# Performance work log

Measured on AMD Instinct MI355X. Metric: run time of the kernel, lower is better.

The kernel has to match this reference:

```python
import jax, jax.numpy as jnp
import numpy as np
from jax import lax

NUM_CLASSES = 10
NUM_ITER = 3
DN = ('NCHW', 'OIHW', 'NCHW')


def squash(t, axis=-1):
    sq = (t ** 2).sum(axis=axis, keepdims=True)
    return (sq / (1.0 + sq)) * t / jnp.sqrt(sq)


def setup_inputs() -> dict:
    key = jax.random.key(0)
    ks = jax.random.split(key, 12)
    B = 512
    s = 0.05  # param scale for numerical stability
    return {
        'x': jax.random.normal(ks[0], (B, 1, 28, 28), jnp.float32),
        'conv1_w': jax.random.normal(ks[1], (256, 1, 9, 9), jnp.float32) * s,
        'conv1_b': jax.random.normal(ks[2], (256,), jnp.float32) * s,
        'prim_w': jax.random.normal(ks[3], (8, 32, 256, 9, 9), jnp.float32) * s,
        'prim_b': jax.random.normal(ks[4], (8, 32), jnp.float32) * s,
        'route_w': jax.random.normal(ks[5], (NUM_CLASSES, 32 * 6 * 6, 8, 16), jnp.float32),
        'dec_w1': jax.random.normal(ks[6], (512, 16 * NUM_CLASSES), jnp.float32) * s,
        'dec_b1': jax.random.normal(ks[7], (512,), jnp.float32) * s,
        'dec_w2': jax.random.normal(ks[8], (1024, 512), jnp.float32) * s,
        'dec_b2': jax.random.normal(ks[9], (1024,), jnp.float32) * s,
        'dec_w3': jax.random.normal(ks[10], (784, 1024), jnp.float32) * s,
        'dec_b3': jax.random.normal(ks[11], (784,), jnp.float32) * s,
    }


def reference(x, conv1_w, conv1_b, prim_w, prim_b, route_w,
              dec_w1, dec_b1, dec_w2, dec_b2, dec_w3, dec_b3):
    B = x.shape[0]
    # conv1 + relu: [B,256,20,20]
    h = lax.conv_general_dilated(x, conv1_w, (1, 1), 'VALID', dimension_numbers=DN)
    h = jax.nn.relu(h + conv1_b[None, :, None, None])
    # primary capsules: 8 parallel convs fused into one conv with 8*32 out channels
    kw = prim_w.reshape(8 * 32, 256, 9, 9)
    u = lax.conv_general_dilated(h, kw, (2, 2), 'VALID', dimension_numbers=DN)
    u = u + prim_b.reshape(-1)[None, :, None, None]          # [B,256,6,6]
    u = u.reshape(B, 8, 32 * 6 * 6).transpose(0, 2, 1)       # [B,1152,8]
    u = squash(u, axis=-1)
    # digit capsules: priors [C,B,R,16]
    priors = jnp.einsum('bri,crio->cbro', u, route_w)
    logits = jnp.zeros_like(priors)
    for i in range(NUM_ITER):
        probs = jax.nn.softmax(logits, axis=2)
        v = squash((probs * priors).sum(axis=2, keepdims=True))  # [C,B,1,16]
        if i != NUM_ITER - 1:
            logits = logits + (priors * v).sum(axis=-1, keepdims=True)
    caps = v.squeeze(2).transpose(1, 0, 2)                    # [B,C,16]
    classes = jnp.sqrt((caps ** 2).sum(axis=-1))              # [B,C]
    classes = jax.nn.softmax(classes, axis=1)
    y = jax.nn.one_hot(jnp.argmax(classes, axis=1), NUM_CLASSES, dtype=caps.dtype)
    d = (caps * y[:, :, None]).reshape(B, -1)                 # [B,160]
    d = jax.nn.relu(d @ dec_w1.T + dec_b1)
    d = jax.nn.relu(d @ dec_w2.T + dec_b2)
    recon = jax.nn.sigmoid(d @ dec_w3.T + dec_b3)             # [B,784]
    return classes, recon
```

## Files before the change

### kernel.cpp

```cpp
#include <hip/hip_runtime.h>
#include <math.h>


typedef _Float16 f16;
typedef _Float16 f16x8 __attribute__((ext_vector_type(8)));
typedef _Float16 f16x4 __attribute__((ext_vector_type(4)));
typedef float f32x4 __attribute__((ext_vector_type(4)));

__device__ __forceinline__ void gl_lds16(const void* g, void* l) {
  __builtin_amdgcn_global_load_lds(
      (const __attribute__((address_space(1))) void*)g,
      (__attribute__((address_space(3))) void*)l, 16, 0, 0);
}

__global__ __launch_bounds__(256, 2) void conv1_kernel(
    const float* __restrict__ x, const float* __restrict__ w,
    const float* __restrict__ bias, f16* __restrict__ ht)
{
  __shared__ float xs[784];
  const int b = blockIdx.x;
  const int t = threadIdx.x;
  for (int i = t; i < 784; i += 256) xs[i] = x[b * 784 + i];
  float wr[81];
#pragma unroll
  for (int k = 0; k < 81; ++k) wr[k] = w[t * 81 + k];
  const float bv = bias[t];
  __syncthreads();
  for (int oy = 0; oy < 20; ++oy) {
    float acc[20];
#pragma unroll
    for (int i = 0; i < 20; ++i) acc[i] = bv;
#pragma unroll
    for (int ky = 0; ky < 9; ++ky) {
      float xr[28];
#pragma unroll
      for (int q = 0; q < 7; ++q) {
        const float4 v = *(const float4*)&xs[(oy + ky) * 28 + q * 4];
        xr[q*4+0] = v.x; xr[q*4+1] = v.y; xr[q*4+2] = v.z; xr[q*4+3] = v.w;
      }
#pragma unroll
      for (int kx = 0; kx < 9; ++kx) {
        const float wv = wr[ky * 9 + kx];
#pragma unroll
        for (int ox = 0; ox < 20; ++ox) acc[ox] = fmaf(xr[ox + kx], wv, acc[ox]);
      }
    }
    f16* hp = &ht[(size_t)((b * 20 + oy) * 20) * 256 + t];
#pragma unroll
    for (int ox = 0; ox < 20; ++ox)
      hp[ox * 256] = (f16)fmaxf(acc[ox], 0.f);
  }
}

__global__ __launch_bounds__(256) void wtrans_kernel(
    const float* __restrict__ w, f16* __restrict__ wt)
{
  __shared__ float tile[64 * 83];
  const int oc = blockIdx.x;
  const int icq = blockIdx.y;
  const int t = threadIdx.x;
  const float* src = w + (size_t)oc * 20736 + (size_t)icq * 64 * 81;
  for (int idx = t; idx < 5184; idx += 256) {
    const int ici = idx / 81, kk = idx - ici * 81;
    tile[ici * 83 + kk] = src[idx];
  }
  __syncthreads();
  f16* dst = wt + (size_t)oc * 20736 + icq * 64;
  for (int idx = t; idx < 5184; idx += 256) {
    const int kk = idx >> 6, ici = idx & 63;
    dst[kk * 256 + ici] = (f16)tile[ici * 83 + kk];
  }
}

__global__ __launch_bounds__(256) void prim_mfma_kernel(
    const f16* __restrict__ ht, const f16* __restrict__ wt,
    float* __restrict__ part)
{
  __shared__ f16 sm[8192];
  const int t = threadIdx.x;
  const int wv = t >> 6, lane = t & 63;
  const int id = blockIdx.x;
  const int g = id >> 3;
  const int mb = (id & 7) + 8 * (g >> 2);
  const int nb = (g >> 1) & 1;
  const int ks = g & 1;
  const int m0 = mb * 128, n0 = nb * 128;

  const int chunk = (lane & 3) ^ ((lane >> 3) & 3);
  long aoff[2], boff[2];
#pragma unroll
  for (int i = 0; i < 2; ++i) {
    const int r = wv * 32 + i * 16 + (lane >> 2);
    const int m = m0 + r;
    const int b = m / 36, pos = m - b * 36;
    const int oy = pos / 6, ox = pos - oy * 6;
    aoff[i] = (long)(((b * 20 + 2 * oy) * 20 + 2 * ox) * 256) * 2 + chunk * 16;
    boff[i] = (long)(n0 + r) * 41472 + chunk * 16;
  }
  const char* htc = (const char*)ht;
  const char* wtc = (const char*)wt;

  const int lrow = lane & 15, quad = lane >> 4;
  const int qx = quad ^ ((lrow >> 1) & 3);
  const int wm = wv & 1, wn = wv >> 1;
  f32x4 acc[4][4] = {};

  const int s0 = ks * 324, s1 = s0 + 324;
  for (int s = s0; s < s1; ++s) {
    const int kykx = s >> 3, icb = s & 7;
    const int ky = kykx / 9, kx = kykx - ky * 9;
    const long astep = (long)((((ky * 20 + kx) * 256) + icb * 32) * 2);
    const long bstep = (long)(((kykx * 256) + icb * 32) * 2);
    __syncthreads();
    {
      char* dA = (char*)sm + wv * 2048;
      char* dB = (char*)sm + 8192 + wv * 2048;
      gl_lds16(htc + aoff[0] + astep, dA);
      gl_lds16(htc + aoff[1] + astep, dA + 1024);
      gl_lds16(wtc + boff[0] + bstep, dB);
      gl_lds16(wtc + boff[1] + bstep, dB + 1024);
    }
    __syncthreads();
    const f16* As = sm;
    const f16* Bs = sm + 4096;
    f16x8 af[4], bf[4];
#pragma unroll
    for (int mt = 0; mt < 4; ++mt)
      af[mt] = *(const f16x8*)&As[(wm * 64 + mt * 16 + lrow) * 32 + qx * 8];
#pragma unroll
    for (int nt = 0; nt < 4; ++nt)
      bf[nt] = *(const f16x8*)&Bs[(wn * 64 + nt * 16 + lrow) * 32 + qx * 8];
#pragma unroll
    for (int mt = 0; mt < 4; ++mt)
#pragma unroll
      for (int nt = 0; nt < 4; ++nt)
        acc[mt][nt] = __builtin_amdgcn_mfma_f32_16x16x32_f16(
            af[mt], bf[nt], acc[mt][nt], 0, 0, 0);
  }

  float* pp = part + (size_t)ks * 4718592;
#pragma unroll
  for (int mt = 0; mt < 4; ++mt) {
    const int mbase = m0 + wm * 64 + mt * 16 + quad * 4;
#pragma unroll
    for (int nt = 0; nt < 4; ++nt) {
      const int n = n0 + wn * 64 + nt * 16 + lrow;
      const int np = (n & 31) * 8 + (n >> 5);
#pragma unroll
      for (int rg = 0; rg < 4; ++rg)
        pp[(size_t)(mbase + rg) * 256 + np] = acc[mt][nt][rg];
    }
  }
}

__global__ void squash_kernel(const float* __restrict__ part,
                              const float* __restrict__ bias,
                              float* __restrict__ u)
{
  const int tid = blockIdx.x * 256 + threadIdx.x;
  if (tid >= 512 * 36 * 32) return;
  const int cc = tid & 31;
  const int row = tid >> 5;
  const int b = row / 36;
  const int pos = row - b * 36;
  const float* p = part + (size_t)row * 256 + cc * 8;
  float v[8] = {};
#pragma unroll
  for (int ksl = 0; ksl < 2; ++ksl) {
    const float4 a0 = *(const float4*)(p + (size_t)ksl * 4718592);
    const float4 a1 = *(const float4*)(p + (size_t)ksl * 4718592 + 4);
    v[0] += a0.x; v[1] += a0.y; v[2] += a0.z; v[3] += a0.w;
    v[4] += a1.x; v[5] += a1.y; v[6] += a1.z; v[7] += a1.w;
  }
  float sq = 0.f;
#pragma unroll
  for (int i = 0; i < 8; ++i) {
    v[i] += bias[i * 32 + cc];
    sq = fmaf(v[i], v[i], sq);
  }
  const float scale = sq / ((1.f + sq) * sqrtf(sq));
  float* up = &u[(size_t)(b * 1152 + cc * 36 + pos) * 8];
#pragma unroll
  for (int i = 0; i < 8; ++i) up[i] = v[i] * scale;
}

__global__ __launch_bounds__(256, 4) void priors_kernel(
    const float* __restrict__ u, const float* __restrict__ rw,
    f16* __restrict__ P)
{
  const int t = threadIdx.x;
  const int rl = t >> 2, oq = t & 3;
  const int r = blockIdx.x * 64 + rl;
  const int b0 = blockIdx.y * 64;
  const int c = blockIdx.z;

  float4 wreg[8];
  const float* wbase = rw + (size_t)(c * 1152 + r) * 128 + oq * 4;
#pragma unroll
  for (int k = 0; k < 8; ++k)
    wreg[k] = *(const float4*)(wbase + k * 16);

  f16* pbase = P + (size_t)((c * 512 + b0) * 1152 + r) * 16 + oq * 4;
  const float* ubase = u + (size_t)(b0 * 1152 + r) * 8;

  for (int b = 0; b < 64; ++b) {
    const float4 ua = *(const float4*)(ubase + (size_t)b * 9216);
    const float4 ub = *(const float4*)(ubase + (size_t)b * 9216 + 4);
    const float uu[8] = {ua.x, ua.y, ua.z, ua.w, ub.x, ub.y, ub.z, ub.w};
    float ax = 0.f, ay = 0.f, az = 0.f, aw = 0.f;
#pragma unroll
    for (int k = 0; k < 8; ++k) {
      ax = fmaf(uu[k], wreg[k].x, ax);
      ay = fmaf(uu[k], wreg[k].y, ay);
      az = fmaf(uu[k], wreg[k].z, az);
      aw = fmaf(uu[k], wreg[k].w, aw);
    }
    f16x4 st;
    st[0] = (f16)ax; st[1] = (f16)ay; st[2] = (f16)az; st[3] = (f16)aw;
    *(f16x4*)(pbase + (size_t)b * 18432) = st;
  }
}

__device__ __forceinline__ float wave_sum(float v) {
#pragma unroll
  for (int off = 32; off > 0; off >>= 1) v += __shfl_xor(v, off);
  return v;
}
__device__ __forceinline__ float wave_max(float v) {
#pragma unroll
  for (int off = 32; off > 0; off >>= 1) v = fmaxf(v, __shfl_xor(v, off));
  return v;
}

__global__ __launch_bounds__(256, 2) void routing_kernel(
    const f16* __restrict__ Pg, float* __restrict__ caps)
{
  const int c = blockIdx.x >> 9;
  const int b = blockIdx.x & 511;
  const int t = threadIdx.x;
  const int wid = t >> 6;
  const int lane = t & 63;
  __shared__ float xred[4 * 17];

  float P[5][16];
  float lg[5];
  const int nk = (t < 128) ? 5 : 4;
#pragma unroll
  for (int k = 0; k < 5; ++k)
#pragma unroll
    for (int o = 0; o < 16; ++o) P[k][o] = 0.f;

  const f16* pbase = Pg + (size_t)((c * 512 + b) * 1152) * 16;
#pragma unroll
  for (int k = 0; k < 5; ++k) {
    if (k < nk) {
      const int r = t + (k << 8);
      const f16x8 p0 = *(const f16x8*)&pbase[(size_t)r * 16];
      const f16x8 p1 = *(const f16x8*)&pbase[(size_t)r * 16 + 8];
#pragma unroll
      for (int o = 0; o < 8; ++o) {
        P[k][o]     = (float)p0[o];
        P[k][o + 8] = (float)p1[o];
      }
    }
  }

  float v[16];
  {
    float sq = 0.f;
#pragma unroll
    for (int o = 0; o < 16; ++o) {
      float p = 0.f;
#pragma unroll
      for (int k = 0; k < 5; ++k) p += P[k][o];
      p = wave_sum(p);
      if (lane == 0) xred[wid * 17 + o] = p;
      v[o] = 0.f;
    }
    __syncthreads();
#pragma unroll
    for (int o = 0; o < 16; ++o) {
      const float s = (xred[o] + xred[17 + o] + xred[34 + o] + xred[51 + o]) *
                      (1.f / 1152.f);
      v[o] = s;
      sq = fmaf(s, s, sq);
    }
    const float scale = sq / ((1.f + sq) * sqrtf(sq));
#pragma unroll
    for (int o = 0; o < 16; ++o) v[o] *= scale;
    __syncthreads();
  }
#pragma unroll
  for (int k = 0; k < 5; ++k) {
    float a = 0.f;
#pragma unroll
    for (int o = 0; o < 16; ++o) a = fmaf(P[k][o], v[o], a);
    lg[k] = a;
  }

  for (int it = 1; it < 3; ++it) {
    float m = -1e30f;
#pragma unroll
    for (int k = 0; k < 5; ++k) if (k < nk) m = fmaxf(m, lg[k]);
    m = wave_max(m);
    if (lane == 0) xred[wid * 17 + 16] = m;
    __syncthreads();
    const float mx = fmaxf(fmaxf(xred[16], xred[17 + 16]),
                           fmaxf(xred[34 + 16], xred[51 + 16]));
    __syncthreads();
    float e[5];
#pragma unroll
    for (int k = 0; k < 5; ++k) e[k] = (k < nk) ? expf(lg[k] - mx) : 0.f;
    float pS = 0.f;
#pragma unroll
    for (int k = 0; k < 5; ++k) pS += e[k];
    pS = wave_sum(pS);
    if (lane == 0) xred[wid * 17 + 16] = pS;
#pragma unroll
    for (int o = 0; o < 16; ++o) {
      float p = 0.f;
#pragma unroll
      for (int k = 0; k < 5; ++k) p = fmaf(e[k], P[k][o], p);
      p = wave_sum(p);
      if (lane == 0) xred[wid * 17 + o] = p;
    }
    __syncthreads();
    const float S = xred[16] + xred[17 + 16] + xred[34 + 16] + xred[51 + 16];
    const float inv = 1.f / S;
    float sq = 0.f;
#pragma unroll
    for (int o = 0; o < 16; ++o) {
      const float s = (xred[o] + xred[17 + o] + xred[34 + o] + xred[51 + o]) * inv;
      v[o] = s;
      sq = fmaf(s, s, sq);
    }
    const float scale = sq / ((1.f + sq) * sqrtf(sq));
#pragma unroll
    for (int o = 0; o < 16; ++o) v[o] *= scale;
    __syncthreads();
    if (it < 2) {
#pragma unroll
      for (int k = 0; k < 5; ++k) {
        float a = 0.f;
#pragma unroll
        for (int o = 0; o < 16; ++o) a = fmaf(P[k][o], v[o], a);
        lg[k] += a;
      }
    }
  }
  if (t == 0) {
    float* cp = &caps[(b * 10 + c) * 16];
#pragma unroll
    for (int o = 0; o < 16; ++o) cp[o] = v[o];
  }
}

__global__ void classes_kernel(const float* __restrict__ caps,
                               float* __restrict__ out_classes,
                               float* __restrict__ d0)
{
  const int b = blockIdx.x * 256 + threadIdx.x;
  if (b >= 512) return;
  float nrm[10];
#pragma unroll
  for (int cc = 0; cc < 10; ++cc) {
    float sq = 0.f;
#pragma unroll
    for (int o = 0; o < 16; ++o) {
      const float vv = caps[(b * 10 + cc) * 16 + o];
      sq = fmaf(vv, vv, sq);
    }
    nrm[cc] = sqrtf(sq);
  }
  float mx = nrm[0]; int cs = 0;
#pragma unroll
  for (int cc = 1; cc < 10; ++cc)
    if (nrm[cc] > mx) { mx = nrm[cc]; cs = cc; }
  float e[10], ssum = 0.f;
#pragma unroll
  for (int cc = 0; cc < 10; ++cc) { e[cc] = expf(nrm[cc] - mx); ssum += e[cc]; }
  const float inv = 1.f / ssum;
#pragma unroll
  for (int cc = 0; cc < 10; ++cc) out_classes[b * 10 + cc] = e[cc] * inv;
#pragma unroll
  for (int cc = 0; cc < 10; ++cc)
#pragma unroll
    for (int o = 0; o < 16; ++o)
      d0[b * 160 + cc * 16 + o] = (cc == cs) ? caps[(b * 10 + cc) * 16 + o] : 0.f;
}

__global__ __launch_bounds__(256, 2) void fc_kernel(
    const float* __restrict__ A, const float* __restrict__ W,
    const float* __restrict__ bias, float* __restrict__ C,
    int N, int K, int act)
{
  __shared__ float As[64][17];
  __shared__ float Ws[64][17];
  const int t = threadIdx.x;
  const int tm = t >> 4, tn = t & 15;
  const int m0 = blockIdx.y << 6, n0 = blockIdx.x << 6;
  const int lr = t >> 2, lq = (t & 3) << 2;
  float acc[4][4] = {};
  for (int k0 = 0; k0 < K; k0 += 16) {
    const float4 av = *(const float4*)&A[(m0 + lr) * K + k0 + lq];
    float4 wv = make_float4(0.f, 0.f, 0.f, 0.f);
    const int wn = n0 + lr;
    if (wn < N) wv = *(const float4*)&W[wn * K + k0 + lq];
    __syncthreads();
    As[lr][lq+0] = av.x; As[lr][lq+1] = av.y; As[lr][lq+2] = av.z; As[lr][lq+3] = av.w;
    Ws[lr][lq+0] = wv.x; Ws[lr][lq+1] = wv.y; Ws[lr][lq+2] = wv.z; Ws[lr][lq+3] = wv.w;
    __syncthreads();
#pragma unroll
    for (int kk = 0; kk < 16; ++kk) {
      float a[4], w[4];
#pragma unroll
      for (int i = 0; i < 4; ++i) a[i] = As[tm * 4 + i][kk];
#pragma unroll
      for (int j = 0; j < 4; ++j) w[j] = Ws[tn * 4 + j][kk];
#pragma unroll
      for (int i = 0; i < 4; ++i)
#pragma unroll
        for (int j = 0; j < 4; ++j) acc[i][j] = fmaf(a[i], w[j], acc[i][j]);
    }
  }
#pragma unroll
  for (int i = 0; i < 4; ++i) {
    const int m = m0 + tm * 4 + i;
#pragma unroll
    for (int j = 0; j < 4; ++j) {
      const int n = n0 + tn * 4 + j;
      if (n < N) {
        float vv = acc[i][j] + bias[n];
        vv = act ? (1.f / (1.f + expf(-vv))) : fmaxf(vv, 0.f);
        C[m * N + n] = vv;
      }
    }
  }
}

extern "C" void kernel_launch(void* const* d_in, const int* in_sizes, int n_in,
                              void* d_out, int out_size, void* d_ws, size_t ws_size,
                              hipStream_t stream)
{
  const float* x       = (const float*)d_in[0];
  const float* conv1_w = (const float*)d_in[1];
  const float* conv1_b = (const float*)d_in[2];
  const float* prim_w  = (const float*)d_in[3];
  const float* prim_b  = (const float*)d_in[4];
  const float* route_w = (const float*)d_in[5];
  const float* dec_w1  = (const float*)d_in[6];
  const float* dec_b1  = (const float*)d_in[7];
  const float* dec_w2  = (const float*)d_in[8];
  const float* dec_b2  = (const float*)d_in[9];
  const float* dec_w3  = (const float*)d_in[10];
  const float* dec_b3  = (const float*)d_in[11];
  float* out = (float*)d_out;

  char* ws = (char*)d_ws;
  f16*   ht   = (f16*)(ws);
  f16*   wtp  = (f16*)(ws + 104857600);
  float* part = (float*)(ws + 115474432);
  float* u    = (float*)(ws + 188743680);
  f16*   P    = (f16*)(ws);
  float* caps = (float*)(ws + 207618048);
  float* d0   = (float*)(ws + 207945728);
  float* d1   = (float*)(ws + 208273408);
  float* d2   = (float*)(ws + 209321984);

  hipLaunchKernelGGL(conv1_kernel, dim3(512), dim3(256), 0, stream,
                     x, conv1_w, conv1_b, ht);
  hipLaunchKernelGGL(wtrans_kernel, dim3(256, 4), dim3(256), 0, stream,
                     prim_w, wtp);
  hipLaunchKernelGGL(prim_mfma_kernel, dim3(576), dim3(256), 0, stream,
                     ht, wtp, part);
  hipLaunchKernelGGL(squash_kernel, dim3(2304), dim3(256), 0, stream,
                     part, prim_b, u);
  hipLaunchKernelGGL(priors_kernel, dim3(18, 8, 10), dim3(256), 0, stream,
                     u, route_w, P);
  hipLaunchKernelGGL(routing_kernel, dim3(5120), dim3(256), 0, stream,
                     P, caps);
  hipLaunchKernelGGL(classes_kernel, dim3(2), dim3(256), 0, stream,
                     caps, out, d0);
  hipLaunchKernelGGL(fc_kernel, dim3(8, 8), dim3(256), 0, stream,
                     d0, dec_w1, dec_b1, d1, 512, 160, 0);
  hipLaunchKernelGGL(fc_kernel, dim3(16, 8), dim3(256), 0, stream,
                     d1, dec_w2, dec_b2, d2, 1024, 512, 0);
  hipLaunchKernelGGL(fc_kernel, dim3(13, 8), dim3(256), 0, stream,
                     d2, dec_w3, dec_b3, out + 5120, 784, 1024, 1);
}
```

Measured before the change: 826.2 us.

## Retile primary-capsule MFMA GEMM to 64x256 tiles with 4-way split-K

The primary-capsule GEMM now uses 64x256 output tiles, so each block covers the full N dimension, and K is split four ways instead of two. This doubles the grid to 1152 blocks, which is meant to improve load balance across CUs and cut the tail wave. In exchange, the partial-sum buffer doubles and squash must reduce four partials, adding global memory traffic. The per-step ratio of MFMA work to LDS loads is also somewhat lower than with 128x128 tiles. Workspace offsets after the partial buffer are shifted to fit the larger buffer.

```diff
diff --git a/kernel.cpp b/kernel.cpp
--- a/kernel.cpp
+++ b/kernel.cpp
@@ -76,36 +76,39 @@
     const f16* __restrict__ ht, const f16* __restrict__ wt,
     float* __restrict__ part)
 {
-  __shared__ f16 sm[8192];
+  __shared__ f16 sm[10240];
+  f16* As = sm;
+  f16* Bs = sm + 2048;
   const int t = threadIdx.x;
   const int wv = t >> 6, lane = t & 63;
   const int id = blockIdx.x;
-  const int g = id >> 3;
-  const int mb = (id & 7) + 8 * (g >> 2);
-  const int nb = (g >> 1) & 1;
-  const int ks = g & 1;
-  const int m0 = mb * 128, n0 = nb * 128;
+  const int ks = (id & 7) >> 1;
+  const int mb = ((id >> 3) << 1) | (id & 1);
+  const int m0 = mb * 64;
 
   const int chunk = (lane & 3) ^ ((lane >> 3) & 3);
-  long aoff[2], boff[2];
-#pragma unroll
-  for (int i = 0; i < 2; ++i) {
-    const int r = wv * 32 + i * 16 + (lane >> 2);
+  long aoff;
+  {
+    const int r = wv * 16 + (lane >> 2);
     const int m = m0 + r;
     const int b = m / 36, pos = m - b * 36;
     const int oy = pos / 6, ox = pos - oy * 6;
-    aoff[i] = (long)(((b * 20 + 2 * oy) * 20 + 2 * ox) * 256) * 2 + chunk * 16;
-    boff[i] = (long)(n0 + r) * 41472 + chunk * 16;
+    aoff = (long)(((b * 20 + 2 * oy) * 20 + 2 * ox) * 256) * 2 + chunk * 16;
+  }
+  long boff[4];
+#pragma unroll
+  for (int i = 0; i < 4; ++i) {
+    const int r = i * 64 + wv * 16 + (lane >> 2);
+    boff[i] = (long)r * 41472 + chunk * 16;
   }
   const char* htc = (const char*)ht;
   const char* wtc = (const char*)wt;
 
   const int lrow = lane & 15, quad = lane >> 4;
   const int qx = quad ^ ((lrow >> 1) & 3);
-  const int wm = wv & 1, wn = wv >> 1;
   f32x4 acc[4][4] = {};
 
-  const int s0 = ks * 324, s1 = s0 + 324;
+  const int s0 = ks * 162, s1 = s0 + 162;
   for (int s = s0; s < s1; ++s) {
     const int kykx = s >> 3, icb = s & 7;
     const int ky = kykx / 9, kx = kykx - ky * 9;
@@ -113,23 +116,19 @@
     const long bstep = (long)(((kykx * 256) + icb * 32) * 2);
     __syncthreads();
     {
-      char* dA = (char*)sm + wv * 2048;
-      char* dB = (char*)sm + 8192 + wv * 2048;
-      gl_lds16(htc + aoff[0] + astep, dA);
-      gl_lds16(htc + aoff[1] + astep, dA + 1024);
-      gl_lds16(wtc + boff[0] + bstep, dB);
-      gl_lds16(wtc + boff[1] + bstep, dB + 1024);
-    }
-    __syncthreads();
-    const f16* As = sm;
-    const f16* Bs = sm + 4096;
+      gl_lds16(htc + aoff + astep, (char*)As + wv * 1024);
+#pragma unroll
+      for (int i = 0; i < 4; ++i)
+        gl_lds16(wtc + boff[i] + bstep, (char*)Bs + i * 4096 + wv * 1024);
+    }
+    __syncthreads();
     f16x8 af[4], bf[4];
 #pragma unroll
     for (int mt = 0; mt < 4; ++mt)
-      af[mt] = *(const f16x8*)&As[(wm * 64 + mt * 16 + lrow) * 32 + qx * 8];
+      af[mt] = *(const f16x8*)&As[(mt * 16 + lrow) * 32 + qx * 8];
 #pragma unroll
     for (int nt = 0; nt < 4; ++nt)
-      bf[nt] = *(const f16x8*)&Bs[(wn * 64 + nt * 16 + lrow) * 32 + qx * 8];
+      bf[nt] = *(const f16x8*)&Bs[(wv * 64 + nt * 16 + lrow) * 32 + qx * 8];
 #pragma unroll
     for (int mt = 0; mt < 4; ++mt)
 #pragma unroll
@@ -141,10 +140,10 @@
   float* pp = part + (size_t)ks * 4718592;
 #pragma unroll
   for (int mt = 0; mt < 4; ++mt) {
-    const int mbase = m0 + wm * 64 + mt * 16 + quad * 4;
+    const int mbase = m0 + mt * 16 + quad * 4;
 #pragma unroll
     for (int nt = 0; nt < 4; ++nt) {
-      const int n = n0 + wn * 64 + nt * 16 + lrow;
+      const int n = wv * 64 + nt * 16 + lrow;
       const int np = (n & 31) * 8 + (n >> 5);
 #pragma unroll
       for (int rg = 0; rg < 4; ++rg)
@@ -166,7 +165,7 @@
   const float* p = part + (size_t)row * 256 + cc * 8;
   float v[8] = {};
 #pragma unroll
-  for (int ksl = 0; ksl < 2; ++ksl) {
+  for (int ksl = 0; ksl < 4; ++ksl) {
     const float4 a0 = *(const float4*)(p + (size_t)ksl * 4718592);
     const float4 a1 = *(const float4*)(p + (size_t)ksl * 4718592 + 4);
     v[0] += a0.x; v[1] += a0.y; v[2] += a0.z; v[3] += a0.w;
@@ -460,18 +459,18 @@
   f16*   ht   = (f16*)(ws);
   f16*   wtp  = (f16*)(ws + 104857600);
   float* part = (float*)(ws + 115474432);
-  float* u    = (float*)(ws + 188743680);
+  float* u    = (float*)(ws + 190971904);
   f16*   P    = (f16*)(ws);
-  float* caps = (float*)(ws + 207618048);
-  float* d0   = (float*)(ws + 207945728);
-  float* d1   = (float*)(ws + 208273408);
-  float* d2   = (float*)(ws + 209321984);
+  float* caps = (float*)(ws + 209846272);
+  float* d0   = (float*)(ws + 210173952);
+  float* d1   = (float*)(ws + 210501632);
+  float* d2   = (float*)(ws + 211550208);
 
   hipLaunchKernelGGL(conv1_kernel, dim3(512), dim3(256), 0, stream,
                      x, conv1_w, conv1_b, ht);
   hipLaunchKernelGGL(wtrans_kernel, dim3(256, 4), dim3(256), 0, stream,
                      prim_w, wtp);
-  hipLaunchKernelGGL(prim_mfma_kernel, dim3(576), dim3(256), 0, stream,
+  hipLaunchKernelGGL(prim_mfma_kernel, dim3(1152), dim3(256), 0, stream,
                      ht, wtp, part);
   hipLaunchKernelGGL(squash_kernel, dim3(2304), dim3(256), 0, stream,
                      part, prim_b, u);
```

Result: slower. 857.3 us (+3.8%).

## Double-buffer primary-capsule MFMA with single-wave tiles; split conv1 rows across blocks

Applied to the files above, without the earlier changes.

The primary-capsule GEMM kernel moves from 256-thread blocks with 128x128 tiles and two barriers per K-step to single-wave 64-thread blocks with 64x64 tiles. Each wave double-buffers its LDS A/B tiles, so the next global-to-LDS load is issued while the current one is consumed by MFMA, and no block barriers are needed. This aims to hide load latency and remove synchronisation stalls, at the cost of more blocks and less operand reuse per tile. Separately, conv1 is split across 4 blocks per image along output rows to give that kernel more parallelism, which means the 81 filter weights are reloaded once per row-group.

```diff
diff --git a/kernel.cpp b/kernel.cpp
--- a/kernel.cpp
+++ b/kernel.cpp
@@ -17,16 +17,17 @@
     const float* __restrict__ x, const float* __restrict__ w,
     const float* __restrict__ bias, f16* __restrict__ ht)
 {
-  __shared__ float xs[784];
+  __shared__ float xs[364];
   const int b = blockIdx.x;
+  const int y0 = blockIdx.y * 5;
   const int t = threadIdx.x;
-  for (int i = t; i < 784; i += 256) xs[i] = x[b * 784 + i];
+  for (int i = t; i < 364; i += 256) xs[i] = x[b * 784 + y0 * 28 + i];
   float wr[81];
 #pragma unroll
   for (int k = 0; k < 81; ++k) wr[k] = w[t * 81 + k];
   const float bv = bias[t];
   __syncthreads();
-  for (int oy = 0; oy < 20; ++oy) {
+  for (int oy = y0; oy < y0 + 5; ++oy) {
     float acc[20];
 #pragma unroll
     for (int i = 0; i < 20; ++i) acc[i] = bv;
@@ -35,7 +36,7 @@
       float xr[28];
 #pragma unroll
       for (int q = 0; q < 7; ++q) {
-        const float4 v = *(const float4*)&xs[(oy + ky) * 28 + q * 4];
+        const float4 v = *(const float4*)&xs[(oy - y0 + ky) * 28 + q * 4];
         xr[q*4+0] = v.x; xr[q*4+1] = v.y; xr[q*4+2] = v.z; xr[q*4+3] = v.w;
       }
 #pragma unroll
@@ -72,83 +73,88 @@
   }
 }
 
-__global__ __launch_bounds__(256) void prim_mfma_kernel(
+__global__ __launch_bounds__(64) void prim_mfma_kernel(
     const f16* __restrict__ ht, const f16* __restrict__ wt,
     float* __restrict__ part)
 {
-  __shared__ f16 sm[8192];
-  const int t = threadIdx.x;
-  const int wv = t >> 6, lane = t & 63;
+  __shared__ f16 A0[2048];
+  __shared__ f16 A1[2048];
+  __shared__ f16 B0[2048];
+  __shared__ f16 B1[2048];
+  const int lane = threadIdx.x;
   const int id = blockIdx.x;
   const int g = id >> 3;
-  const int mb = (id & 7) + 8 * (g >> 2);
-  const int nb = (g >> 1) & 1;
   const int ks = g & 1;
-  const int m0 = mb * 128, n0 = nb * 128;
+  const int nt = (g >> 1) & 3;
+  const int mt = (id & 7) + 8 * (g >> 3);
+  const int m0 = mt * 64, n0 = nt * 64;
 
   const int chunk = (lane & 3) ^ ((lane >> 3) & 3);
-  long aoff[2], boff[2];
-#pragma unroll
-  for (int i = 0; i < 2; ++i) {
-    const int r = wv * 32 + i * 16 + (lane >> 2);
-    const int m = m0 + r;
+  long aoff[4], boff[4];
+#pragma unroll
+  for (int i = 0; i < 4; ++i) {
+    const int row = i * 16 + (lane >> 2);
+    const int m = m0 + row;
     const int b = m / 36, pos = m - b * 36;
     const int oy = pos / 6, ox = pos - oy * 6;
     aoff[i] = (long)(((b * 20 + 2 * oy) * 20 + 2 * ox) * 256) * 2 + chunk * 16;
-    boff[i] = (long)(n0 + r) * 41472 + chunk * 16;
+    boff[i] = (long)(n0 + row) * 41472 + chunk * 16;
   }
   const char* htc = (const char*)ht;
   const char* wtc = (const char*)wt;
 
   const int lrow = lane & 15, quad = lane >> 4;
-  const int qx = quad ^ ((lrow >> 1) & 3);
-  const int wm = wv & 1, wn = wv >> 1;
+  const int cp = quad ^ ((lrow >> 1) & 3);
   f32x4 acc[4][4] = {};
 
   const int s0 = ks * 324, s1 = s0 + 324;
-  for (int s = s0; s < s1; ++s) {
-    const int kykx = s >> 3, icb = s & 7;
-    const int ky = kykx / 9, kx = kykx - ky * 9;
-    const long astep = (long)((((ky * 20 + kx) * 256) + icb * 32) * 2);
-    const long bstep = (long)(((kykx * 256) + icb * 32) * 2);
-    __syncthreads();
-    {
-      char* dA = (char*)sm + wv * 2048;
-      char* dB = (char*)sm + 8192 + wv * 2048;
-      gl_lds16(htc + aoff[0] + astep, dA);
-      gl_lds16(htc + aoff[1] + astep, dA + 1024);
-      gl_lds16(wtc + boff[0] + bstep, dB);
-      gl_lds16(wtc + boff[1] + bstep, dB + 1024);
-    }
-    __syncthreads();
-    const f16* As = sm;
-    const f16* Bs = sm + 4096;
-    f16x8 af[4], bf[4];
-#pragma unroll
-    for (int mt = 0; mt < 4; ++mt)
-      af[mt] = *(const f16x8*)&As[(wm * 64 + mt * 16 + lrow) * 32 + qx * 8];
-#pragma unroll
-    for (int nt = 0; nt < 4; ++nt)
-      bf[nt] = *(const f16x8*)&Bs[(wn * 64 + nt * 16 + lrow) * 32 + qx * 8];
-#pragma unroll
-    for (int mt = 0; mt < 4; ++mt)
-#pragma unroll
-      for (int nt = 0; nt < 4; ++nt)
-        acc[mt][nt] = __builtin_amdgcn_mfma_f32_16x16x32_f16(
-            af[mt], bf[nt], acc[mt][nt], 0, 0, 0);
-  }
+
+#define STAGE(S, AB, BB)                                                      \
+  {                                                                           \
+    const int kykx = (S) >> 3, icb = (S) & 7;                                 \
+    const int ky = kykx / 9, kx = kykx - ky * 9;                              \
+    const long astep = (long)((((ky * 20 + kx) * 256) + icb * 32) * 2);       \
+    const long bstep = (long)(((kykx * 256) + icb * 32) * 2);                 \
+    _Pragma("unroll") for (int i = 0; i < 4; ++i) {                           \
+      gl_lds16(htc + aoff[i] + astep, (char*)(AB) + i * 1024);                \
+      gl_lds16(wtc + boff[i] + bstep, (char*)(BB) + i * 1024);                \
+    }                                                                         \
+  }
+
+#define CONSUME(AB, BB)                                                       \
+  {                                                                           \
+    f16x8 af[4], bf[4];                                                       \
+    _Pragma("unroll") for (int m4 = 0; m4 < 4; ++m4)                          \
+        af[m4] = *(const f16x8*)&(AB)[(m4 * 16 + lrow) * 32 + cp * 8];        \
+    _Pragma("unroll") for (int n4 = 0; n4 < 4; ++n4)                          \
+        bf[n4] = *(const f16x8*)&(BB)[(n4 * 16 + lrow) * 32 + cp * 8];        \
+    _Pragma("unroll") for (int m4 = 0; m4 < 4; ++m4)                          \
+        _Pragma("unroll") for (int n4 = 0; n4 < 4; ++n4)                      \
+            acc[m4][n4] = __builtin_amdgcn_mfma_f32_16x16x32_f16(             \
+                af[m4], bf[n4], acc[m4][n4], 0, 0, 0);                        \
+  }
+
+  STAGE(s0, A0, B0);
+  for (int s = s0; s < s1; s += 2) {
+    STAGE(s + 1, A1, B1);
+    CONSUME(A0, B0);
+    if (s + 2 < s1) STAGE(s + 2, A0, B0);
+    CONSUME(A1, B1);
+  }
+#undef STAGE
+#undef CONSUME
 
   float* pp = part + (size_t)ks * 4718592;
 #pragma unroll
-  for (int mt = 0; mt < 4; ++mt) {
-    const int mbase = m0 + wm * 64 + mt * 16 + quad * 4;
-#pragma unroll
-    for (int nt = 0; nt < 4; ++nt) {
-      const int n = n0 + wn * 64 + nt * 16 + lrow;
+  for (int m4 = 0; m4 < 4; ++m4) {
+    const int mbase = m0 + m4 * 16 + quad * 4;
+#pragma unroll
+    for (int n4 = 0; n4 < 4; ++n4) {
+      const int n = n0 + n4 * 16 + lrow;
       const int np = (n & 31) * 8 + (n >> 5);
 #pragma unroll
       for (int rg = 0; rg < 4; ++rg)
-        pp[(size_t)(mbase + rg) * 256 + np] = acc[mt][nt][rg];
+        pp[(size_t)(mbase + rg) * 256 + np] = acc[m4][n4][rg];
     }
   }
 }
@@ -467,11 +473,11 @@
   float* d1   = (float*)(ws + 208273408);
   float* d2   = (float*)(ws + 209321984);
 
-  hipLaunchKernelGGL(conv1_kernel, dim3(512), dim3(256), 0, stream,
+  hipLaunchKernelGGL(conv1_kernel, dim3(512, 4), dim3(256), 0, stream,
                      x, conv1_w, conv1_b, ht);
   hipLaunchKernelGGL(wtrans_kernel, dim3(256, 4), dim3(256), 0, stream,
                      prim_w, wtp);
-  hipLaunchKernelGGL(prim_mfma_kernel, dim3(576), dim3(256), 0, stream,
+  hipLaunchKernelGGL(prim_mfma_kernel, dim3(2304), dim3(64), 0, stream,
                      ht, wtp, part);
   hipLaunchKernelGGL(squash_kernel, dim3(2304), dim3(256), 0, stream,
                      part, prim_b, u);
```

Result: slower. 931.0 us (+12.7%).
